# Kernel tuning notes

Measured on AMD Instinct MI355X. Metric: run time of the kernel, lower is better.

Reference implementation:

```python
import jax, jax.numpy as jnp
import numpy as np

EPS = 1e-7
B, C, IMG = 1024, 3, 32
NCLASS = 10
N_IN, L_IN, L_OUT = 64, 16, 16   # primary caps: 64 capsules of length 16; digit caps length 16
R_ITER = 3


def squash(c, axis):
    dot = jnp.sum(c * c, axis=axis, keepdims=True)
    return dot / (1.0 + dot) / jnp.sqrt(dot + EPS) * c


def conv2d(x, w, b, stride):
    y = jax.lax.conv_general_dilated(x, w, (stride, stride), 'VALID',
                                     dimension_numbers=('NCHW', 'OIHW', 'NCHW'))
    return y + b[None, :, None, None]


def setup_inputs() -> dict:
    key = jax.random.key(0)
    ks = jax.random.split(key, 16)
    inp = {
        'x': jax.random.uniform(ks[0], (B, C, IMG, IMG), dtype=jnp.float32),
        'y': jax.random.randint(ks[1], (B,), 0, NCLASS, dtype=jnp.int64),
        'conv1_w': 0.05 * jax.random.normal(ks[2], (128, C, 3, 3), jnp.float32),
        'conv1_b': jnp.zeros((128,), jnp.float32),
        'conv2_w': 0.05 * jax.random.normal(ks[3], (256, 128, 5, 5), jnp.float32),
        'conv2_b': jnp.zeros((256,), jnp.float32),
        'conv3_w': 0.05 * jax.random.normal(ks[4], (256, 256, 5, 5), jnp.float32),
        'conv3_b': jnp.zeros((256,), jnp.float32),
        'caps_w': 0.05 * jax.random.normal(ks[5], (N_IN, NCLASS, L_IN, L_OUT), jnp.float32),
        'caps_b': 0.05 * jax.random.normal(ks[6], (NCLASS, L_OUT), jnp.float32),
        'fc1_w': 0.05 * jax.random.normal(ks[7], (512, NCLASS * L_OUT), jnp.float32),
        'fc1_b': jnp.zeros((512,), jnp.float32),
        'fc2_w': 0.05 * jax.random.normal(ks[8], (1024, 512), jnp.float32),
        'fc2_b': jnp.zeros((1024,), jnp.float32),
        'fc3_w': 0.05 * jax.random.normal(ks[9], (IMG * IMG * C, 1024), jnp.float32),
        'fc3_b': jnp.zeros((IMG * IMG * C,), jnp.float32),
    }
    return inp


def reference(x, y, conv1_w, conv1_b, conv2_w, conv2_b, conv3_w, conv3_b,
              caps_w, caps_b, fc1_w, fc1_b, fc2_w, fc2_b, fc3_w, fc3_b):
    # CNN blocks
    h = jax.nn.relu(conv2d(x, conv1_w, conv1_b, 2))   # [B,128,15,15]
    h = jax.nn.relu(conv2d(h, conv2_w, conv2_b, 2))   # [B,256,6,6]
    h = jax.nn.relu(conv2d(h, conv3_w, conv3_b, 1))   # [B,256,2,2]

    # Primary capsules: [B,64,16], squashed along capsule-length axis
    prim = squash(h.reshape(h.shape[0], N_IN, L_IN), axis=-1)

    # u_hat[b,i,o,j] = sum_k W[i,o,k,j] * prim[b,i,k]  -> [B,64,10,16]
    u_hat = jnp.einsum('bik,iokj->bioj', prim, caps_w)
    u_hat_det = jax.lax.stop_gradient(u_hat)

    b_ij = jnp.zeros((h.shape[0], N_IN, NCLASS), dtype=u_hat.dtype)
    v = None
    for r in range(R_ITER):
        c_ij = jax.nn.softmax(b_ij, axis=2)           # over output capsules
        uh = u_hat if r == R_ITER - 1 else u_hat_det
        s = jnp.einsum('bio,bioj->boj', c_ij, uh) + caps_b   # [B,10,16]
        v = squash(s, axis=-1)
        if r < R_ITER - 1:
            agree = jnp.einsum('bioj,boj->bio', u_hat_det, jax.lax.stop_gradient(v))
            b_ij = b_ij + agree

    # capsule lengths: [B,10,1,1]
    v_lengths = jnp.sqrt(jnp.sum(v * v, axis=-1, keepdims=True) + EPS)[..., None]

    # reconstruction (mask by true label one-hot)
    one_hot = jax.nn.one_hot(y, NCLASS, dtype=v.dtype)       # [B,10]
    masked = (v * one_hot[:, :, None]).reshape(v.shape[0], NCLASS * L_OUT)
    h1 = jax.nn.relu(masked @ fc1_w.T + fc1_b)
    h2 = jax.nn.relu(h1 @ fc2_w.T + fc2_b)
    decoded = jax.nn.sigmoid(h2 @ fc3_w.T + fc3_b)           # [B,3072]
    return (v_lengths, decoded)
```

## Files before the change

kernel.cpp:

```cpp
#include <hip/hip_runtime.h>
#include <hip/hip_bf16.h>
#include <math.h>

#define EPSF 1e-7f

typedef __attribute__((ext_vector_type(8))) short bhalf8;
typedef __attribute__((ext_vector_type(4))) float floatx4;

__global__ __launch_bounds__(256) void conv1_kernel(
    const float* __restrict__ x, const float* __restrict__ w,
    const float* __restrict__ bias, __hip_bfloat16* __restrict__ out)
{
  __shared__ float wl[3456];
  __shared__ float bl[128];
  const int b = blockIdx.x;
  const int t = threadIdx.x;
  for (int i = t; i < 3456; i += 256) wl[i] = w[i];
  if (t < 128) bl[t] = bias[t];
  __syncthreads();
  if (t >= 225) return;
  const int py = t / 15, px = t % 15;
  const float* xb = x + b * 3072;
  float win[27];
#pragma unroll
  for (int c = 0; c < 3; ++c)
#pragma unroll
    for (int ky = 0; ky < 3; ++ky)
#pragma unroll
      for (int kx = 0; kx < 3; ++kx)
        win[c*9 + ky*3 + kx] = xb[c*1024 + (py*2 + ky)*32 + (px*2 + kx)];
#pragma unroll 1
  for (int oc0 = 0; oc0 < 128; oc0 += 32) {
    __hip_bfloat16 hv[32];
#pragma unroll
    for (int oc = 0; oc < 32; ++oc) {
      const float* wp = &wl[(oc0 + oc)*27];
      float acc = bl[oc0 + oc];
#pragma unroll
      for (int q = 0; q < 27; ++q) acc = fmaf(win[q], wp[q], acc);
      hv[oc] = __float2bfloat16(fmaxf(acc, 0.f));
    }
    uint4* dst = (uint4*)&out[((size_t)b*225 + t)*128 + oc0];
    const uint4* src = (const uint4*)hv;
#pragma unroll
    for (int q = 0; q < 4; ++q) dst[q] = src[q];
  }
}

__global__ __launch_bounds__(256) void prep_kernel(
    const float* __restrict__ conv2w, const float* __restrict__ conv3w,
    const float* __restrict__ capsw,  const float* __restrict__ fc1w,
    const float* __restrict__ fc2w,   const float* __restrict__ fc3w,
    __hip_bfloat16* __restrict__ wt2, __hip_bfloat16* __restrict__ wt3,
    __hip_bfloat16* __restrict__ cwt, float* __restrict__ fc1wt,
    __hip_bfloat16* __restrict__ wf2, __hip_bfloat16* __restrict__ wf3)
{
  const int t = threadIdx.x;
  int b = blockIdx.x;
  if (b < 12288) {
    int i = b*256 + t;
    wf3[i] = __float2bfloat16(fc3w[i]);
    return;
  }
  b -= 12288;
  if (b < 6400) {
    int i = b*256 + t;
    int s = i >> 14, r = i & 16383;
    int oc = r >> 6, kq = r & 63;
    int k = s*64 + kq;
    int tap = k >> 8, ic = k & 255;
    wt3[i] = __float2bfloat16(conv3w[(oc*256 + ic)*25 + tap]);
    return;
  }
  b -= 6400;
  if (b < 3200) {
    int i = b*256 + t;
    int s = i >> 13, r = i & 8191;
    int oc = r >> 5, kq = r & 31;
    int h = (s >= 50) ? 1 : 0;
    int r2 = s - h*50;
    int tap = r2 >> 1, q = r2 & 1;
    int ic = h*64 + q*32 + kq;
    wt2[i] = __float2bfloat16(conv2w[(oc*128 + ic)*25 + tap]);
    return;
  }
  b -= 3200;
  if (b < 2048) {
    int i = b*256 + t;
    wf2[i] = __float2bfloat16(fc2w[i]);
    return;
  }
  b -= 2048;
  if (b < 640) {
    int i2 = b*256 + t;
    int k = i2 & 15, j = (i2 >> 4) & 15, io = i2 >> 8;
    cwt[i2] = __float2bfloat16(capsw[(io*16 + k)*16 + j]);
    return;
  }
  b -= 640;
  {
    int i = b*256 + t;
    int j = i >> 9, n = i & 511;
    fc1wt[i] = fc1w[n*160 + j];
  }
}

__global__ __launch_bounds__(1024) void conv2_mfma_kernel(
    const __hip_bfloat16* __restrict__ a,
    const __hip_bfloat16* __restrict__ wt,
    const float* __restrict__ bias,
    __hip_bfloat16* __restrict__ out)
{
  __shared__ __align__(16) unsigned short Il[4*225*64];
  const int b0   = blockIdx.x * 4;
  const int t    = threadIdx.x;
  const int lane = t & 63;
  const int w    = t >> 6;
  const int wm   = w >> 3;
  const int wn   = w & 7;
  const int n    = lane & 15;
  const int g    = lane >> 4;

  const char* gB = (const char*)wt + (wn*32 + n)*64 + g*16;
  bhalf8 b00 = *(const bhalf8*)(gB);
  bhalf8 b01 = *(const bhalf8*)(gB + 1024);
  bhalf8 b10 = *(const bhalf8*)(gB + 16384);
  bhalf8 b11 = *(const bhalf8*)(gB + 16384 + 1024);

  int Abase[5], em[5];
#pragma unroll
  for (int mt = 0; mt < 5; ++mt) {
    int tile = wm*5 + mt;
    int m = tile*16 + n;
    if (m >= 144) m = 0;
    int img = m / 36, pos = m - img*36;
    int py = pos / 6, px = pos - py*6;
    int pixb = 30*py + 2*px;
    Abase[mt] = (img*225 + pixb) * 128;
    em[mt] = g + m;
  }

  floatx4 acc[5][2];
#pragma unroll
  for (int mt = 0; mt < 5; ++mt)
#pragma unroll
    for (int nt = 0; nt < 2; ++nt)
      acc[mt][nt] = (floatx4){0.f, 0.f, 0.f, 0.f};

  int s = 0;
#pragma unroll 1
  for (int h = 0; h < 2; ++h) {
    if (h) __syncthreads();
    for (int i = t; i < 7200; i += 1024) {
      int img = i / 1800;
      int r = i - img*1800;
      int p = r >> 3, c = r & 7;
      uint4 v = *(const uint4*)((const char*)a +
                ((size_t)(b0+img)*225 + p)*256 + h*128 + c*16);
      int px15 = p % 15, py15 = p / 15;
      int csw = (c + (px15 >> 1) + 6*(py15 >> 1) + ((img & 1) << 2)) & 7;
      *(uint4*)((char*)Il + (img*225 + p)*128 + csw*16) = v;
    }
    __syncthreads();

    int dpix = 0, kx = 0, ky = 0;
#pragma unroll 1
    for (int tap = 0; tap < 25; ++tap) {
      const int doff = dpix << 7;
      const int dsw  = (kx >> 1) + 6*(ky >> 1);
      int a0[5];
#pragma unroll
      for (int mt = 0; mt < 5; ++mt)
        a0[mt] = Abase[mt] + doff + (((em[mt] + dsw) & 7) << 4);

#pragma unroll
      for (int mt = 0; mt < 4; ++mt) {
        bhalf8 av = *(const bhalf8*)((const char*)Il + a0[mt]);
        acc[mt][0] = __builtin_amdgcn_mfma_f32_16x16x32_bf16(av, b00, acc[mt][0], 0, 0, 0);
        acc[mt][1] = __builtin_amdgcn_mfma_f32_16x16x32_bf16(av, b01, acc[mt][1], 0, 0, 0);
      }
      if (wm == 0) {
        bhalf8 av = *(const bhalf8*)((const char*)Il + a0[4]);
        acc[4][0] = __builtin_amdgcn_mfma_f32_16x16x32_bf16(av, b00, acc[4][0], 0, 0, 0);
        acc[4][1] = __builtin_amdgcn_mfma_f32_16x16x32_bf16(av, b01, acc[4][1], 0, 0, 0);
      }
      {
        const int spre = (s + 2 < 100) ? (s + 2) : 99;
        b00 = *(const bhalf8*)(gB + (size_t)spre*16384);
        b01 = *(const bhalf8*)(gB + (size_t)spre*16384 + 1024);
      }
#pragma unroll
      for (int mt = 0; mt < 4; ++mt) {
        bhalf8 av = *(const bhalf8*)((const char*)Il + (a0[mt] ^ 64));
        acc[mt][0] = __builtin_amdgcn_mfma_f32_16x16x32_bf16(av, b10, acc[mt][0], 0, 0, 0);
        acc[mt][1] = __builtin_amdgcn_mfma_f32_16x16x32_bf16(av, b11, acc[mt][1], 0, 0, 0);
      }
      if (wm == 0) {
        bhalf8 av = *(const bhalf8*)((const char*)Il + (a0[4] ^ 64));
        acc[4][0] = __builtin_amdgcn_mfma_f32_16x16x32_bf16(av, b10, acc[4][0], 0, 0, 0);
        acc[4][1] = __builtin_amdgcn_mfma_f32_16x16x32_bf16(av, b11, acc[4][1], 0, 0, 0);
      }
      {
        const int spre = (s + 3 < 100) ? (s + 3) : 99;
        b10 = *(const bhalf8*)(gB + (size_t)spre*16384);
        b11 = *(const bhalf8*)(gB + (size_t)spre*16384 + 1024);
      }
      s += 2;
      if (kx == 4) { kx = 0; ++ky; dpix += 11; } else { ++kx; ++dpix; }
    }
  }

  const float bv0 = bias[wn*32 + n];
  const float bv1 = bias[wn*32 + 16 + n];
#pragma unroll
  for (int mt = 0; mt < 5; ++mt) {
    if (mt < 4 || wm == 0) {
      int tile = wm*5 + mt;
#pragma unroll
      for (int r = 0; r < 4; ++r) {
        int m = tile*16 + g*4 + r;
        int img = m / 36, pos = m - img*36;
        size_t o = (((size_t)(b0+img)*36 + pos) << 8) + wn*32 + n;
        out[o]      = __float2bfloat16(fmaxf(acc[mt][0][r] + bv0, 0.f));
        out[o + 16] = __float2bfloat16(fmaxf(acc[mt][1][r] + bv1, 0.f));
      }
    }
  }
}

__global__ __launch_bounds__(512) void conv3_mfma_kernel(
    const __hip_bfloat16* __restrict__ a,
    const __hip_bfloat16* __restrict__ wt,
    float* __restrict__ pout)
{
  __shared__ __align__(16) unsigned short Il[16*1448];
  const int b0   = blockIdx.x * 16;
  const int kq   = blockIdx.y;
  const int t    = threadIdx.x;
  const int lane = t & 63;
  const int w    = t >> 6;
  const int n    = lane & 15;
  const int g    = lane >> 4;

  for (int i = t; i < 2304; i += 512) {
    int img = i / 144, r = i - img*144;
    int p = r >> 2, c = r & 3;
    uint4 v = *(const uint4*)((const char*)a +
              ((((size_t)(b0+img)*36 + p) << 9) + kq*64 + c*16));
    *(uint4*)((char*)Il + (img*1448 + p*40 + c*8)*2) = v;
  }

  const char* gB = (const char*)wt + (size_t)(w*32 + n)*128 +
                   (kq & 1)*64 + g*16;
  const int kqs = kq >> 1;
  bhalf8 b00, b01, b10, b11;
  b00 = *(const bhalf8*)(gB + (size_t)(0*4 + kqs)*32768);
  b01 = *(const bhalf8*)(gB + (size_t)(0*4 + kqs)*32768 + 2048);
  b10 = *(const bhalf8*)(gB + (size_t)(1*4 + kqs)*32768);
  b11 = *(const bhalf8*)(gB + (size_t)(1*4 + kqs)*32768 + 2048);

  const int d = n >> 2, pos = n & 3;
  const int pb = (pos >> 1)*6 + (pos & 1);
  int ab[4];
#pragma unroll
  for (int mt = 0; mt < 4; ++mt)
    ab[mt] = ((mt*4 + d)*1448 + pb*40 + g*8) * 2;

  floatx4 acc[4][2];
#pragma unroll
  for (int mt = 0; mt < 4; ++mt)
#pragma unroll
    for (int nt = 0; nt < 2; ++nt)
      acc[mt][nt] = (floatx4){0.f, 0.f, 0.f, 0.f};

  __syncthreads();

  int toff = 0, kx = 0;
#pragma unroll 1
  for (int tap = 0; tap < 24; tap += 2) {
#pragma unroll
    for (int mt = 0; mt < 4; ++mt) {
      bhalf8 av = *(const bhalf8*)((const char*)Il + ab[mt] + toff*80);
      acc[mt][0] = __builtin_amdgcn_mfma_f32_16x16x32_bf16(av, b00, acc[mt][0], 0, 0, 0);
      acc[mt][1] = __builtin_amdgcn_mfma_f32_16x16x32_bf16(av, b01, acc[mt][1], 0, 0, 0);
    }
    b00 = *(const bhalf8*)(gB + (size_t)((tap+2)*4 + kqs)*32768);
    b01 = *(const bhalf8*)(gB + (size_t)((tap+2)*4 + kqs)*32768 + 2048);
    if (++kx == 5) { kx = 0; toff += 2; } else ++toff;
#pragma unroll
    for (int mt = 0; mt < 4; ++mt) {
      bhalf8 av = *(const bhalf8*)((const char*)Il + ab[mt] + toff*80);
      acc[mt][0] = __builtin_amdgcn_mfma_f32_16x16x32_bf16(av, b10, acc[mt][0], 0, 0, 0);
      acc[mt][1] = __builtin_amdgcn_mfma_f32_16x16x32_bf16(av, b11, acc[mt][1], 0, 0, 0);
    }
    {
      const int tpre = (tap + 3 <= 24) ? (tap + 3) : 24;
      b10 = *(const bhalf8*)(gB + (size_t)(tpre*4 + kqs)*32768);
      b11 = *(const bhalf8*)(gB + (size_t)(tpre*4 + kqs)*32768 + 2048);
    }
    if (++kx == 5) { kx = 0; toff += 2; } else ++toff;
  }
#pragma unroll
  for (int mt = 0; mt < 4; ++mt) {
    bhalf8 av = *(const bhalf8*)((const char*)Il + ab[mt] + toff*80);
    acc[mt][0] = __builtin_amdgcn_mfma_f32_16x16x32_bf16(av, b00, acc[mt][0], 0, 0, 0);
    acc[mt][1] = __builtin_amdgcn_mfma_f32_16x16x32_bf16(av, b01, acc[mt][1], 0, 0, 0);
  }

  float* po = pout + (size_t)kq*1048576;
#pragma unroll
  for (int mt = 0; mt < 4; ++mt) {
#pragma unroll
    for (int r = 0; r < 4; ++r) {
      int m = mt*16 + g*4 + r;
      int img = m >> 2, p2 = m & 3;
#pragma unroll
      for (int nt = 0; nt < 2; ++nt)
        po[((size_t)(b0+img)*256 + w*32 + nt*16 + n)*4 + p2] = acc[mt][nt][r];
    }
  }
}

__global__ __launch_bounds__(256) void caps_kernel(
    const float* __restrict__ pout, const __hip_bfloat16* __restrict__ cwt,
    const float* __restrict__ cb, const float* __restrict__ c3b,
    const int* __restrict__ y,
    const float* __restrict__ fc1wt, const float* __restrict__ fc1b,
    float* __restrict__ vlen, __hip_bfloat16* __restrict__ h1f)
{
  __shared__ float prim[1024];
  __shared__ float uh[10240];
  __shared__ float bij[640];
  __shared__ float cij[640];
  __shared__ float vv[160];
  const int b = blockIdx.x, t = threadIdx.x;
  {
    const float* pp = pout + (size_t)b*1024 + t*4;
    float4 s4 = *(const float4*)pp;
#pragma unroll
    for (int q = 1; q < 8; ++q) {
      float4 v = *(const float4*)(pp + (size_t)q*1048576);
      s4.x += v.x; s4.y += v.y; s4.z += v.z; s4.w += v.w;
    }
    const float bv = c3b[t];
    float4 h = make_float4(fmaxf(s4.x + bv, 0.f), fmaxf(s4.y + bv, 0.f),
                           fmaxf(s4.z + bv, 0.f), fmaxf(s4.w + bv, 0.f));
    float dd = h.x*h.x + h.y*h.y + h.z*h.z + h.w*h.w;
    dd += __shfl_xor(dd, 1);
    dd += __shfl_xor(dd, 2);
    float sc = dd / (1.f + dd) / sqrtf(dd + EPSF);
    float4 o4 = make_float4(h.x*sc, h.y*sc, h.z*sc, h.w*sc);
    *(float4*)&prim[t*4] = o4;
  }
  for (int f = t; f < 640; f += 256) bij[f] = 0.f;
  __syncthreads();
  for (int f = t; f < 10240; f += 256) {
    const int i = f / 160;
    const uint4* wv = (const uint4*)(cwt + (size_t)f*16);
    uint4 wa = wv[0], wb = wv[1];
    unsigned uw[8] = {wa.x, wa.y, wa.z, wa.w, wb.x, wb.y, wb.z, wb.w};
    const float* pp = prim + i*16;
    float s = 0.f;
#pragma unroll
    for (int q = 0; q < 8; ++q) {
      float lo = __uint_as_float(uw[q] << 16);
      float hi = __uint_as_float(uw[q] & 0xffff0000u);
      s = fmaf(pp[2*q],   lo, s);
      s = fmaf(pp[2*q+1], hi, s);
    }
    uh[f] = s;
  }
  __syncthreads();
  for (int r = 0; r < 3; ++r) {
    if (t < 64) {
      float e[10];
      float mx = -1e30f;
#pragma unroll
      for (int o = 0; o < 10; ++o) { e[o] = bij[t*10 + o]; mx = fmaxf(mx, e[o]); }
      float sum = 0.f;
#pragma unroll
      for (int o = 0; o < 10; ++o) { e[o] = expf(e[o] - mx); sum += e[o]; }
      float inv = 1.f / sum;
#pragma unroll
      for (int o = 0; o < 10; ++o) cij[t*10 + o] = e[o] * inv;
    }
    __syncthreads();
    if (t < 160) {
      const int o = t >> 4;
      float s = cb[t];
      for (int i = 0; i < 64; ++i) s = fmaf(cij[i*10 + o], uh[i*160 + t], s);
      float dd = s*s;
      dd += __shfl_xor(dd, 1); dd += __shfl_xor(dd, 2);
      dd += __shfl_xor(dd, 4); dd += __shfl_xor(dd, 8);
      float sc = dd / (1.f + dd) / sqrtf(dd + EPSF);
      vv[t] = s * sc;
      if (r == 2 && (t & 15) == 0)
        vlen[b*10 + o] = sqrtf(sc*sc*dd + EPSF);
    }
    __syncthreads();
    if (r < 2) {
      for (int f = t; f < 640; f += 256) {
        int i = f / 10, o = f % 10;
        const float* up = &uh[i*160 + o*16];
        const float* vp = &vv[o*16];
        float a = 0.f;
#pragma unroll
        for (int j = 0; j < 16; ++j) a = fmaf(up[j], vp[j], a);
        bij[f] += a;
      }
      __syncthreads();
    }
  }
  const int yb = y[b];
  const float* vy = &vv[yb*16];
  for (int nn = t; nn < 512; nn += 256) {
    float s = fc1b[nn];
#pragma unroll
    for (int k = 0; k < 16; ++k)
      s = fmaf(vy[k], fc1wt[(yb*16 + k)*512 + nn], s);
    h1f[b*512 + nn] = __float2bfloat16(fmaxf(s, 0.f));
  }
}

template<int ACT, int MT, int NT>
__global__ __launch_bounds__(256) void fc_mfma_kernel(
    const __hip_bfloat16* __restrict__ A,
    const __hip_bfloat16* __restrict__ W,
    const float* __restrict__ bias,
    void* __restrict__ outv, int M, int N, int K)
{
  const int t    = threadIdx.x;
  const int lane = t & 63;
  const int w    = t >> 6;
  const int wr   = w >> 1, wc = w & 1;
  const int n    = lane & 15, g = lane >> 4;
  const int m0   = blockIdx.x * (2*MT*16) + wr*(MT*16);
  const int n0   = blockIdx.y * (2*NT*16) + wc*(NT*16);
  const __hip_bfloat16* Ap = A + (size_t)(m0 + n)*K + g*8;
  const __hip_bfloat16* Wp = W + (size_t)(n0 + n)*K + g*8;
  const int steps = K >> 5;

  bhalf8 aa0[MT], aa1[MT], bb0[NT], bb1[NT];
#pragma unroll
  for (int mt = 0; mt < MT; ++mt) {
    aa0[mt] = *(const bhalf8*)(Ap + (size_t)mt*16*K);
    aa1[mt] = *(const bhalf8*)(Ap + (size_t)mt*16*K + 32);
  }
#pragma unroll
  for (int nt = 0; nt < NT; ++nt) {
    bb0[nt] = *(const bhalf8*)(Wp + (size_t)nt*16*K);
    bb1[nt] = *(const bhalf8*)(Wp + (size_t)nt*16*K + 32);
  }

  floatx4 acc[MT][NT];
#pragma unroll
  for (int mt = 0; mt < MT; ++mt)
#pragma unroll
    for (int nt = 0; nt < NT; ++nt)
      acc[mt][nt] = (floatx4){0.f, 0.f, 0.f, 0.f};

#pragma unroll 1
  for (int s = 0; s < steps; s += 2) {
#pragma unroll
    for (int mt = 0; mt < MT; ++mt)
#pragma unroll
      for (int nt = 0; nt < NT; ++nt)
        acc[mt][nt] = __builtin_amdgcn_mfma_f32_16x16x32_bf16(
            aa0[mt], bb0[nt], acc[mt][nt], 0, 0, 0);
    {
      const int spre = (s + 2 < steps) ? (s + 2) : s;
#pragma unroll
      for (int mt = 0; mt < MT; ++mt)
        aa0[mt] = *(const bhalf8*)(Ap + (size_t)mt*16*K + spre*32);
#pragma unroll
      for (int nt = 0; nt < NT; ++nt)
        bb0[nt] = *(const bhalf8*)(Wp + (size_t)nt*16*K + spre*32);
    }
#pragma unroll
    for (int mt = 0; mt < MT; ++mt)
#pragma unroll
      for (int nt = 0; nt < NT; ++nt)
        acc[mt][nt] = __builtin_amdgcn_mfma_f32_16x16x32_bf16(
            aa1[mt], bb1[nt], acc[mt][nt], 0, 0, 0);
    {
      const int spre = (s + 3 < steps) ? (s + 3) : (s + 1);
#pragma unroll
      for (int mt = 0; mt < MT; ++mt)
        aa1[mt] = *(const bhalf8*)(Ap + (size_t)mt*16*K + spre*32);
#pragma unroll
      for (int nt = 0; nt < NT; ++nt)
        bb1[nt] = *(const bhalf8*)(Wp + (size_t)nt*16*K + spre*32);
    }
  }

#pragma unroll
  for (int mt = 0; mt < MT; ++mt) {
#pragma unroll
    for (int r = 0; r < 4; ++r) {
      const int m = m0 + mt*16 + g*4 + r;
#pragma unroll
      for (int nt = 0; nt < NT; ++nt) {
        const int col = n0 + nt*16 + n;
        float v = acc[mt][nt][r] + bias[col];
        if (ACT == 0) {
          ((__hip_bfloat16*)outv)[(size_t)m*N + col] =
              __float2bfloat16(fmaxf(v, 0.f));
        } else {
          ((float*)outv)[(size_t)m*N + col] = 1.f / (1.f + expf(-v));
        }
      }
    }
  }
}

extern "C" void kernel_launch(void* const* d_in, const int* in_sizes, int n_in,
                              void* d_out, int out_size, void* d_ws, size_t ws_size,
                              hipStream_t stream) {
  const float* x       = (const float*)d_in[0];
  const int*   y       = (const int*)  d_in[1];
  const float* conv1_w = (const float*)d_in[2];
  const float* conv1_b = (const float*)d_in[3];
  const float* conv2_w = (const float*)d_in[4];
  const float* conv2_b = (const float*)d_in[5];
  const float* conv3_w = (const float*)d_in[6];
  const float* conv3_b = (const float*)d_in[7];
  const float* caps_w  = (const float*)d_in[8];
  const float* caps_b  = (const float*)d_in[9];
  const float* fc1_w   = (const float*)d_in[10];
  const float* fc1_b   = (const float*)d_in[11];
  const float* fc2_w   = (const float*)d_in[12];
  const float* fc2_b   = (const float*)d_in[13];
  const float* fc3_w   = (const float*)d_in[14];
  const float* fc3_b   = (const float*)d_in[15];
  float* out = (float*)d_out;
  float* ws  = (float*)d_ws;

  __hip_bfloat16* h1t   = (__hip_bfloat16*)ws;
  __hip_bfloat16* wt2   = (__hip_bfloat16*)(ws + 14745600);
  __hip_bfloat16* wt3   = (__hip_bfloat16*)(ws + 15155200);
  __hip_bfloat16* h2t   = (__hip_bfloat16*)(ws + 15974400);
  float*          pout  = ws + 20692992;
  __hip_bfloat16* h1f   = (__hip_bfloat16*)(ws + 29081600);
  __hip_bfloat16* h2f   = (__hip_bfloat16*)(ws + 29343744);
  __hip_bfloat16* wf2   = (__hip_bfloat16*)(ws + 29868032);
  __hip_bfloat16* wf3   = (__hip_bfloat16*)(ws + 30130176);
  __hip_bfloat16* cwt   = (__hip_bfloat16*)(ws + 31703040);
  float*          fc1wt = ws + 31784960;

  prep_kernel<<<dim3(24896), 256, 0, stream>>>(
      conv2_w, conv3_w, caps_w, fc1_w, fc2_w, fc3_w,
      wt2, wt3, cwt, fc1wt, wf2, wf3);
  conv1_kernel<<<dim3(1024),       256, 0, stream>>>(x, conv1_w, conv1_b, h1t);
  conv2_mfma_kernel<<<dim3(256),  1024, 0, stream>>>(h1t, wt2, conv2_b, h2t);
  conv3_mfma_kernel<<<dim3(64, 8), 512, 0, stream>>>(h2t, wt3, pout);
  caps_kernel<<<dim3(1024),        256, 0, stream>>>(pout, cwt, caps_b, conv3_b,
                                                     y, fc1wt, fc1_b, out, h1f);
  fc_mfma_kernel<0,2,2><<<dim3(16, 16), 256, 0, stream>>>(
      h1f, wf2, fc2_b, h2f, 1024, 1024, 512);
  fc_mfma_kernel<1,2,2><<<dim3(16, 48), 256, 0, stream>>>(
      h2f, wf3, fc3_b, out + 10240, 1024, 3072, 1024);
}
```

Before: 340.4 us.

## Widen conv2 warp N-tile, drop conv1 LDS weights, split caps accumulators

Measured after the change: 352.8 us. +3.7%, slower.

```diff
diff --git a/kernel.cpp b/kernel.cpp
--- a/kernel.cpp
+++ b/kernel.cpp
@@ -11,13 +11,8 @@
     const float* __restrict__ x, const float* __restrict__ w,
     const float* __restrict__ bias, __hip_bfloat16* __restrict__ out)
 {
-  __shared__ float wl[3456];
-  __shared__ float bl[128];
   const int b = blockIdx.x;
   const int t = threadIdx.x;
-  for (int i = t; i < 3456; i += 256) wl[i] = w[i];
-  if (t < 128) bl[t] = bias[t];
-  __syncthreads();
   if (t >= 225) return;
   const int py = t / 15, px = t % 15;
   const float* xb = x + b * 3072;
@@ -34,8 +29,8 @@
     __hip_bfloat16 hv[32];
 #pragma unroll
     for (int oc = 0; oc < 32; ++oc) {
-      const float* wp = &wl[(oc0 + oc)*27];
-      float acc = bl[oc0 + oc];
+      const float* wp = &w[(oc0 + oc)*27];
+      float acc = bias[oc0 + oc];
 #pragma unroll
       for (int q = 0; q < 27; ++q) acc = fmaf(win[q], wp[q], acc);
       hv[oc] = __float2bfloat16(fmaxf(acc, 0.f));
@@ -105,7 +100,7 @@
   }
 }
 
-__global__ __launch_bounds__(1024) void conv2_mfma_kernel(
+__global__ __launch_bounds__(512) void conv2_mfma_kernel(
     const __hip_bfloat16* __restrict__ a,
     const __hip_bfloat16* __restrict__ wt,
     const float* __restrict__ bias,
@@ -116,16 +111,18 @@
   const int t    = threadIdx.x;
   const int lane = t & 63;
   const int w    = t >> 6;
-  const int wm   = w >> 3;
-  const int wn   = w & 7;
+  const int wm   = w >> 2;
+  const int wn   = w & 3;
   const int n    = lane & 15;
   const int g    = lane >> 4;
 
-  const char* gB = (const char*)wt + (wn*32 + n)*64 + g*16;
-  bhalf8 b00 = *(const bhalf8*)(gB);
-  bhalf8 b01 = *(const bhalf8*)(gB + 1024);
-  bhalf8 b10 = *(const bhalf8*)(gB + 16384);
-  bhalf8 b11 = *(const bhalf8*)(gB + 16384 + 1024);
+  const char* gB = (const char*)wt + (wn*64 + n)*64 + g*16;
+  bhalf8 bs0[4], bs1[4];
+#pragma unroll
+  for (int nt = 0; nt < 4; ++nt) {
+    bs0[nt] = *(const bhalf8*)(gB + nt*1024);
+    bs1[nt] = *(const bhalf8*)(gB + 16384 + nt*1024);
+  }
 
   int Abase[5], em[5];
 #pragma unroll
@@ -140,18 +137,18 @@
     em[mt] = g + m;
   }
 
-  floatx4 acc[5][2];
+  floatx4 acc[5][4];
 #pragma unroll
   for (int mt = 0; mt < 5; ++mt)
 #pragma unroll
-    for (int nt = 0; nt < 2; ++nt)
+    for (int nt = 0; nt < 4; ++nt)
       acc[mt][nt] = (floatx4){0.f, 0.f, 0.f, 0.f};
 
   int s = 0;
 #pragma unroll 1
   for (int h = 0; h < 2; ++h) {
     if (h) __syncthreads();
-    for (int i = t; i < 7200; i += 1024) {
+    for (int i = t; i < 7200; i += 512) {
       int img = i / 1800;
       int r = i - img*1800;
       int p = r >> 3, c = r & 7;
@@ -176,42 +173,49 @@
 #pragma unroll
       for (int mt = 0; mt < 4; ++mt) {
         bhalf8 av = *(const bhalf8*)((const char*)Il + a0[mt]);
-        acc[mt][0] = __builtin_amdgcn_mfma_f32_16x16x32_bf16(av, b00, acc[mt][0], 0, 0, 0);
-        acc[mt][1] = __builtin_amdgcn_mfma_f32_16x16x32_bf16(av, b01, acc[mt][1], 0, 0, 0);
+#pragma unroll
+        for (int nt = 0; nt < 4; ++nt)
+          acc[mt][nt] = __builtin_amdgcn_mfma_f32_16x16x32_bf16(av, bs0[nt], acc[mt][nt], 0, 0, 0);
       }
       if (wm == 0) {
         bhalf8 av = *(const bhalf8*)((const char*)Il + a0[4]);
-        acc[4][0] = __builtin_amdgcn_mfma_f32_16x16x32_bf16(av, b00, acc[4][0], 0, 0, 0);
-        acc[4][1] = __builtin_amdgcn_mfma_f32_16x16x32_bf16(av, b01, acc[4][1], 0, 0, 0);
+#pragma unroll
+        for (int nt = 0; nt < 4; ++nt)
+          acc[4][nt] = __builtin_amdgcn_mfma_f32_16x16x32_bf16(av, bs0[nt], acc[4][nt], 0, 0, 0);
       }
       {
         const int spre = (s + 2 < 100) ? (s + 2) : 99;
-        b00 = *(const bhalf8*)(gB + (size_t)spre*16384);
-        b01 = *(const bhalf8*)(gB + (size_t)spre*16384 + 1024);
+#pragma unroll
+        for (int nt = 0; nt < 4; ++nt)
+          bs0[nt] = *(const bhalf8*)(gB + (size_t)spre*16384 + nt*1024);
       }
 #pragma unroll
       for (int mt = 0; mt < 4; ++mt) {
         bhalf8 av = *(const bhalf8*)((const char*)Il + (a0[mt] ^ 64));
-        acc[mt][0] = __builtin_amdgcn_mfma_f32_16x16x32_bf16(av, b10, acc[mt][0], 0, 0, 0);
-        acc[mt][1] = __builtin_amdgcn_mfma_f32_16x16x32_bf16(av, b11, acc[mt][1], 0, 0, 0);
+#pragma unroll
+        for (int nt = 0; nt < 4; ++nt)
+          acc[mt][nt] = __builtin_amdgcn_mfma_f32_16x16x32_bf16(av, bs1[nt], acc[mt][nt], 0, 0, 0);
       }
       if (wm == 0) {
         bhalf8 av = *(const bhalf8*)((const char*)Il + (a0[4] ^ 64));
-        acc[4][0] = __builtin_amdgcn_mfma_f32_16x16x32_bf16(av, b10, acc[4][0], 0, 0, 0);
-        acc[4][1] = __builtin_amdgcn_mfma_f32_16x16x32_bf16(av, b11, acc[4][1], 0, 0, 0);
+#pragma unroll
+        for (int nt = 0; nt < 4; ++nt)
+          acc[4][nt] = __builtin_amdgcn_mfma_f32_16x16x32_bf16(av, bs1[nt], acc[4][nt], 0, 0, 0);
       }
       {
         const int spre = (s + 3 < 100) ? (s + 3) : 99;
-        b10 = *(const bhalf8*)(gB + (size_t)spre*16384);
-        b11 = *(const bhalf8*)(gB + (size_t)spre*16384 + 1024);
+#pragma unroll
+        for (int nt = 0; nt < 4; ++nt)
+          bs1[nt] = *(const bhalf8*)(gB + (size_t)spre*16384 + nt*1024);
       }
       s += 2;
       if (kx == 4) { kx = 0; ++ky; dpix += 11; } else { ++kx; ++dpix; }
     }
   }
 
-  const float bv0 = bias[wn*32 + n];
-  const float bv1 = bias[wn*32 + 16 + n];
+  float bv[4];
+#pragma unroll
+  for (int nt = 0; nt < 4; ++nt) bv[nt] = bias[wn*64 + nt*16 + n];
 #pragma unroll
   for (int mt = 0; mt < 5; ++mt) {
     if (mt < 4 || wm == 0) {
@@ -220,9 +224,10 @@
       for (int r = 0; r < 4; ++r) {
         int m = tile*16 + g*4 + r;
         int img = m / 36, pos = m - img*36;
-        size_t o = (((size_t)(b0+img)*36 + pos) << 8) + wn*32 + n;
-        out[o]      = __float2bfloat16(fmaxf(acc[mt][0][r] + bv0, 0.f));
-        out[o + 16] = __float2bfloat16(fmaxf(acc[mt][1][r] + bv1, 0.f));
+        size_t o = (((size_t)(b0+img)*36 + pos) << 8) + wn*64 + n;
+#pragma unroll
+        for (int nt = 0; nt < 4; ++nt)
+          out[o + nt*16] = __float2bfloat16(fmaxf(acc[mt][nt][r] + bv[nt], 0.f));
       }
     }
   }
@@ -387,8 +392,14 @@
     __syncthreads();
     if (t < 160) {
       const int o = t >> 4;
-      float s = cb[t];
-      for (int i = 0; i < 64; ++i) s = fmaf(cij[i*10 + o], uh[i*160 + t], s);
+      float s0 = cb[t], s1 = 0.f, s2 = 0.f, s3 = 0.f;
+      for (int i = 0; i < 64; i += 4) {
+        s0 = fmaf(cij[(i+0)*10 + o], uh[(i+0)*160 + t], s0);
+        s1 = fmaf(cij[(i+1)*10 + o], uh[(i+1)*160 + t], s1);
+        s2 = fmaf(cij[(i+2)*10 + o], uh[(i+2)*160 + t], s2);
+        s3 = fmaf(cij[(i+3)*10 + o], uh[(i+3)*160 + t], s3);
+      }
+      float s = (s0 + s1) + (s2 + s3);
       float dd = s*s;
       dd += __shfl_xor(dd, 1); dd += __shfl_xor(dd, 2);
       dd += __shfl_xor(dd, 4); dd += __shfl_xor(dd, 8);
@@ -551,7 +562,7 @@
       conv2_w, conv3_w, caps_w, fc1_w, fc2_w, fc3_w,
       wt2, wt3, cwt, fc1wt, wf2, wf3);
   conv1_kernel<<<dim3(1024),       256, 0, stream>>>(x, conv1_w, conv1_b, h1t);
-  conv2_mfma_kernel<<<dim3(256),  1024, 0, stream>>>(h1t, wt2, conv2_b, h2t);
+  conv2_mfma_kernel<<<dim3(256),   512, 0, stream>>>(h1t, wt2, conv2_b, h2t);
   conv3_mfma_kernel<<<dim3(64, 8), 512, 0, stream>>>(h2t, wt3, pout);
   caps_kernel<<<dim3(1024),        256, 0, stream>>>(pout, cwt, caps_b, conv3_b,
                                                      y, fc1wt, fc1_b, out, h1f);
```

## Batch conv1 over two images, deepen conv2 weight prefetch, split caps reductions

Applied to the files above, without the earlier changes.

Measured after the change: 425.7 us. 1.25x slower.

```diff
diff --git a/kernel.cpp b/kernel.cpp
--- a/kernel.cpp
+++ b/kernel.cpp
@@ -11,39 +11,58 @@
     const float* __restrict__ x, const float* __restrict__ w,
     const float* __restrict__ bias, __hip_bfloat16* __restrict__ out)
 {
-  __shared__ float wl[3456];
+  __shared__ float wl[4096];
   __shared__ float bl[128];
-  const int b = blockIdx.x;
+  const int b0 = blockIdx.x * 2;
   const int t = threadIdx.x;
-  for (int i = t; i < 3456; i += 256) wl[i] = w[i];
+  for (int i = t; i < 4096; i += 256) {
+    int oc = i >> 5, q = i & 31;
+    wl[i] = (q < 27) ? w[oc*27 + q] : 0.f;
+  }
   if (t < 128) bl[t] = bias[t];
   __syncthreads();
   if (t >= 225) return;
   const int py = t / 15, px = t % 15;
-  const float* xb = x + b * 3072;
-  float win[27];
-#pragma unroll
-  for (int c = 0; c < 3; ++c)
-#pragma unroll
-    for (int ky = 0; ky < 3; ++ky)
-#pragma unroll
-      for (int kx = 0; kx < 3; ++kx)
-        win[c*9 + ky*3 + kx] = xb[c*1024 + (py*2 + ky)*32 + (px*2 + kx)];
+  float win[2][28];
+  win[0][27] = 0.f; win[1][27] = 0.f;
+#pragma unroll
+  for (int im = 0; im < 2; ++im) {
+    const float* xb = x + (size_t)(b0 + im) * 3072;
+#pragma unroll
+    for (int c = 0; c < 3; ++c)
+#pragma unroll
+      for (int ky = 0; ky < 3; ++ky)
+#pragma unroll
+        for (int kx = 0; kx < 3; ++kx)
+          win[im][c*9 + ky*3 + kx] = xb[c*1024 + (py*2 + ky)*32 + (px*2 + kx)];
+  }
 #pragma unroll 1
   for (int oc0 = 0; oc0 < 128; oc0 += 32) {
-    __hip_bfloat16 hv[32];
+    __hip_bfloat16 hv[2][32];
 #pragma unroll
     for (int oc = 0; oc < 32; ++oc) {
-      const float* wp = &wl[(oc0 + oc)*27];
-      float acc = bl[oc0 + oc];
-#pragma unroll
-      for (int q = 0; q < 27; ++q) acc = fmaf(win[q], wp[q], acc);
-      hv[oc] = __float2bfloat16(fmaxf(acc, 0.f));
-    }
-    uint4* dst = (uint4*)&out[((size_t)b*225 + t)*128 + oc0];
-    const uint4* src = (const uint4*)hv;
-#pragma unroll
-    for (int q = 0; q < 4; ++q) dst[q] = src[q];
+      const float4* wp = (const float4*)&wl[(oc0 + oc) << 5];
+      float a0 = bl[oc0 + oc], a1 = a0;
+#pragma unroll
+      for (int qq = 0; qq < 7; ++qq) {
+        float4 wv = wp[qq];
+        a0 = fmaf(win[0][qq*4+0], wv.x, a0); a1 = fmaf(win[1][qq*4+0], wv.x, a1);
+        a0 = fmaf(win[0][qq*4+1], wv.y, a0); a1 = fmaf(win[1][qq*4+1], wv.y, a1);
+        a0 = fmaf(win[0][qq*4+2], wv.z, a0); a1 = fmaf(win[1][qq*4+2], wv.z, a1);
+        a0 = fmaf(win[0][qq*4+3], wv.w, a0); a1 = fmaf(win[1][qq*4+3], wv.w, a1);
+      }
+      hv[0][oc] = __float2bfloat16(fmaxf(a0, 0.f));
+      hv[1][oc] = __float2bfloat16(fmaxf(a1, 0.f));
+    }
+#pragma unroll
+    for (int qq = 0; qq < 4; ++qq) {
+      int c16 = (oc0 >> 3) + qq;
+#pragma unroll
+      for (int im = 0; im < 2; ++im) {
+        const uint4* src = (const uint4*)hv[im];
+        *(uint4*)((char*)out + (size_t)(b0+im)*57600 + c16*3600 + t*16) = src[qq];
+      }
+    }
   }
 }
 
@@ -104,6 +123,50 @@
     fc1wt[i] = fc1w[n*160 + j];
   }
 }
+
+#define C2_TAP(QA0,QA1,QB0,QB1)                                               \
+  {                                                                           \
+    const int doff = dpix << 7;                                               \
+    const int dsw  = (kx >> 1) + 6*(ky >> 1);                                 \
+    int a0[5];                                                                \
+    _Pragma("unroll")                                                         \
+    for (int mt = 0; mt < 5; ++mt)                                            \
+      a0[mt] = Abase[mt] + doff + (((em[mt] + dsw) & 7) << 4);                \
+    _Pragma("unroll")                                                         \
+    for (int mt = 0; mt < 4; ++mt) {                                          \
+      bhalf8 av = *(const bhalf8*)((const char*)Il + a0[mt]);                 \
+      acc[mt][0] = __builtin_amdgcn_mfma_f32_16x16x32_bf16(av, QA0, acc[mt][0], 0, 0, 0); \
+      acc[mt][1] = __builtin_amdgcn_mfma_f32_16x16x32_bf16(av, QA1, acc[mt][1], 0, 0, 0); \
+    }                                                                         \
+    if (wm == 0) {                                                            \
+      bhalf8 av = *(const bhalf8*)((const char*)Il + a0[4]);                  \
+      acc[4][0] = __builtin_amdgcn_mfma_f32_16x16x32_bf16(av, QA0, acc[4][0], 0, 0, 0); \
+      acc[4][1] = __builtin_amdgcn_mfma_f32_16x16x32_bf16(av, QA1, acc[4][1], 0, 0, 0); \
+    }                                                                         \
+    {                                                                         \
+      const int spre = (s + 4 < 100) ? (s + 4) : 99;                          \
+      QA0 = *(const bhalf8*)(gB + (size_t)spre*16384);                        \
+      QA1 = *(const bhalf8*)(gB + (size_t)spre*16384 + 1024);                 \
+    }                                                                         \
+    _Pragma("unroll")                                                         \
+    for (int mt = 0; mt < 4; ++mt) {                                          \
+      bhalf8 av = *(const bhalf8*)((const char*)Il + (a0[mt] ^ 64));          \
+      acc[mt][0] = __builtin_amdgcn_mfma_f32_16x16x32_bf16(av, QB0, acc[mt][0], 0, 0, 0); \
+      acc[mt][1] = __builtin_amdgcn_mfma_f32_16x16x32_bf16(av, QB1, acc[mt][1], 0, 0, 0); \
+    }                                                                         \
+    if (wm == 0) {                                                            \
+      bhalf8 av = *(const bhalf8*)((const char*)Il + (a0[4] ^ 64));           \
+      acc[4][0] = __builtin_amdgcn_mfma_f32_16x16x32_bf16(av, QB0, acc[4][0], 0, 0, 0); \
+      acc[4][1] = __builtin_amdgcn_mfma_f32_16x16x32_bf16(av, QB1, acc[4][1], 0, 0, 0); \
+    }                                                                         \
+    {                                                                         \
+      const int spre = (s + 5 < 100) ? (s + 5) : 99;                          \
+      QB0 = *(const bhalf8*)(gB + (size_t)spre*16384);                        \
+      QB1 = *(const bhalf8*)(gB + (size_t)spre*16384 + 1024);                 \
+    }                                                                         \
+    s += 2;                                                                   \
+    if (kx == 4) { kx = 0; ++ky; dpix += 11; } else { ++kx; ++dpix; }         \
+  }
 
 __global__ __launch_bounds__(1024) void conv2_mfma_kernel(
     const __hip_bfloat16* __restrict__ a,
@@ -122,10 +185,14 @@
   const int g    = lane >> 4;
 
   const char* gB = (const char*)wt + (wn*32 + n)*64 + g*16;
-  bhalf8 b00 = *(const bhalf8*)(gB);
-  bhalf8 b01 = *(const bhalf8*)(gB + 1024);
-  bhalf8 b10 = *(const bhalf8*)(gB + 16384);
-  bhalf8 b11 = *(const bhalf8*)(gB + 16384 + 1024);
+  bhalf8 bA0 = *(const bhalf8*)(gB);
+  bhalf8 bA1 = *(const bhalf8*)(gB + 1024);
+  bhalf8 bB0 = *(const bhalf8*)(gB + 1*16384);
+  bhalf8 bB1 = *(const bhalf8*)(gB + 1*16384 + 1024);
+  bhalf8 bC0 = *(const bhalf8*)(gB + 2*16384);
+  bhalf8 bC1 = *(const bhalf8*)(gB + 2*16384 + 1024);
+  bhalf8 bD0 = *(const bhalf8*)(gB + 3*16384);
+  bhalf8 bD1 = *(const bhalf8*)(gB + 3*16384 + 1024);
 
   int Abase[5], em[5];
 #pragma unroll
@@ -156,7 +223,7 @@
       int r = i - img*1800;
       int p = r >> 3, c = r & 7;
       uint4 v = *(const uint4*)((const char*)a +
-                ((size_t)(b0+img)*225 + p)*256 + h*128 + c*16);
+                (size_t)(b0+img)*57600 + (h*8 + c)*3600 + p*16);
       int px15 = p % 15, py15 = p / 15;
       int csw = (c + (px15 >> 1) + 6*(py15 >> 1) + ((img & 1) << 2)) & 7;
       *(uint4*)((char*)Il + (img*225 + p)*128 + csw*16) = v;
@@ -164,49 +231,20 @@
     __syncthreads();
 
     int dpix = 0, kx = 0, ky = 0;
+    if (h == 0) {
 #pragma unroll 1
-    for (int tap = 0; tap < 25; ++tap) {
-      const int doff = dpix << 7;
-      const int dsw  = (kx >> 1) + 6*(ky >> 1);
-      int a0[5];
-#pragma unroll
-      for (int mt = 0; mt < 5; ++mt)
-        a0[mt] = Abase[mt] + doff + (((em[mt] + dsw) & 7) << 4);
-
-#pragma unroll
-      for (int mt = 0; mt < 4; ++mt) {
-        bhalf8 av = *(const bhalf8*)((const char*)Il + a0[mt]);
-        acc[mt][0] = __builtin_amdgcn_mfma_f32_16x16x32_bf16(av, b00, acc[mt][0], 0, 0, 0);
-        acc[mt][1] = __builtin_amdgcn_mfma_f32_16x16x32_bf16(av, b01, acc[mt][1], 0, 0, 0);
-      }
-      if (wm == 0) {
-        bhalf8 av = *(const bhalf8*)((const char*)Il + a0[4]);
-        acc[4][0] = __builtin_amdgcn_mfma_f32_16x16x32_bf16(av, b00, acc[4][0], 0, 0, 0);
-        acc[4][1] = __builtin_amdgcn_mfma_f32_16x16x32_bf16(av, b01, acc[4][1], 0, 0, 0);
-      }
-      {
-        const int spre = (s + 2 < 100) ? (s + 2) : 99;
-        b00 = *(const bhalf8*)(gB + (size_t)spre*16384);
-        b01 = *(const bhalf8*)(gB + (size_t)spre*16384 + 1024);
-      }
-#pragma unroll
-      for (int mt = 0; mt < 4; ++mt) {
-        bhalf8 av = *(const bhalf8*)((const char*)Il + (a0[mt] ^ 64));
-        acc[mt][0] = __builtin_amdgcn_mfma_f32_16x16x32_bf16(av, b10, acc[mt][0], 0, 0, 0);
-        acc[mt][1] = __builtin_amdgcn_mfma_f32_16x16x32_bf16(av, b11, acc[mt][1], 0, 0, 0);
-      }
-      if (wm == 0) {
-        bhalf8 av = *(const bhalf8*)((const char*)Il + (a0[4] ^ 64));
-        acc[4][0] = __builtin_amdgcn_mfma_f32_16x16x32_bf16(av, b10, acc[4][0], 0, 0, 0);
-        acc[4][1] = __builtin_amdgcn_mfma_f32_16x16x32_bf16(av, b11, acc[4][1], 0, 0, 0);
-      }
-      {
-        const int spre = (s + 3 < 100) ? (s + 3) : 99;
-        b10 = *(const bhalf8*)(gB + (size_t)spre*16384);
-        b11 = *(const bhalf8*)(gB + (size_t)spre*16384 + 1024);
-      }
-      s += 2;
-      if (kx == 4) { kx = 0; ++ky; dpix += 11; } else { ++kx; ++dpix; }
+      for (int tp = 0; tp < 12; ++tp) {
+        C2_TAP(bA0,bA1,bB0,bB1);
+        C2_TAP(bC0,bC1,bD0,bD1);
+      }
+      C2_TAP(bA0,bA1,bB0,bB1);
+    } else {
+#pragma unroll 1
+      for (int tp = 0; tp < 12; ++tp) {
+        C2_TAP(bC0,bC1,bD0,bD1);
+        C2_TAP(bA0,bA1,bB0,bB1);
+      }
+      C2_TAP(bC0,bC1,bD0,bD1);
     }
   }
 
@@ -387,8 +425,14 @@
     __syncthreads();
     if (t < 160) {
       const int o = t >> 4;
-      float s = cb[t];
-      for (int i = 0; i < 64; ++i) s = fmaf(cij[i*10 + o], uh[i*160 + t], s);
+      float s0 = cb[t], s1 = 0.f, s2 = 0.f, s3 = 0.f;
+      for (int i = 0; i < 64; i += 4) {
+        s0 = fmaf(cij[(i+0)*10 + o], uh[(i+0)*160 + t], s0);
+        s1 = fmaf(cij[(i+1)*10 + o], uh[(i+1)*160 + t], s1);
+        s2 = fmaf(cij[(i+2)*10 + o], uh[(i+2)*160 + t], s2);
+        s3 = fmaf(cij[(i+3)*10 + o], uh[(i+3)*160 + t], s3);
+      }
+      float s = (s0 + s1) + (s2 + s3);
       float dd = s*s;
       dd += __shfl_xor(dd, 1); dd += __shfl_xor(dd, 2);
       dd += __shfl_xor(dd, 4); dd += __shfl_xor(dd, 8);
@@ -550,7 +594,7 @@
   prep_kernel<<<dim3(24896), 256, 0, stream>>>(
       conv2_w, conv3_w, caps_w, fc1_w, fc2_w, fc3_w,
       wt2, wt3, cwt, fc1wt, wf2, wf3);
-  conv1_kernel<<<dim3(1024),       256, 0, stream>>>(x, conv1_w, conv1_b, h1t);
+  conv1_kernel<<<dim3(512),        256, 0, stream>>>(x, conv1_w, conv1_b, h1t);
   conv2_mfma_kernel<<<dim3(256),  1024, 0, stream>>>(h1t, wt2, conv2_b, h2t);
   conv3_mfma_kernel<<<dim3(64, 8), 512, 0, stream>>>(h2t, wt3, pout);
   caps_kernel<<<dim3(1024),        256, 0, stream>>>(pout, cwt, caps_b, conv3_b,
```
